# Kernel tuning notes

Measured on AMD Instinct MI355X. Metric: run time of the kernel, lower is better.

The kernel has to match this reference:

```python
import jax, jax.numpy as jnp
import numpy as np

NUM_HEADS = 4
D_K = 64
D_MODEL = NUM_HEADS * D_K  # 256
SEN_LEN = 8192
N_GROUPS = 4096
BASE_LEN = 64
N_EDGES = N_GROUPS * BASE_LEN  # 262144
PATH_LEN = 64


def setup_inputs() -> dict:
    rng = np.random.default_rng(0)
    key = jax.random.key(0)
    ks = jax.random.split(key, 16)

    # ragged group lengths, each >= 2, summing exactly to N_EDGES
    half = N_GROUPS // 2
    r = rng.integers(-(BASE_LEN - 2), BASE_LEN - 1, size=half)
    edge_len = np.concatenate([BASE_LEN + r, BASE_LEN - r]).astype(np.int64)
    assert edge_len.sum() == N_EDGES and edge_len.min() >= 2

    # distinct token ids; include src=0 and tar=1 so path_agg branches fire
    perm = rng.permutation(np.arange(2, SEN_LEN))[: N_GROUPS - 2]
    token_ids = np.concatenate([np.array([0, 1]), perm]).astype(np.int64)

    def w(k, shape):
        return jax.random.normal(k, shape, jnp.float32) / np.sqrt(shape[-1]).astype(np.float32)

    return {
        "path": jax.random.normal(ks[0], (PATH_LEN, D_MODEL), jnp.float32),
        "path_len": PATH_LEN,
        "q": jax.random.normal(ks[1], (SEN_LEN, D_MODEL), jnp.float32),
        "k": jax.random.normal(ks[2], (N_EDGES, D_MODEL), jnp.float32),
        "v": jax.random.normal(ks[3], (N_EDGES, D_MODEL), jnp.float32),
        "graphs": 0,
        "edge_len": jnp.asarray(edge_len),
        "token_ids": jnp.asarray(token_ids),
        "pair": jnp.array([0, 1], jnp.int32),
        "rev": 0,
        "W_qpair": w(ks[4], (D_MODEL, 2 * D_MODEL)),
        "W_pk": w(ks[5], (D_MODEL, D_MODEL)),
        "W_pv": w(ks[6], (D_MODEL, D_MODEL)),
        "W_q": w(ks[7], (D_MODEL, D_MODEL)),
        "W_k": w(ks[8], (D_MODEL, D_MODEL)),
        "W_v": w(ks[9], (D_MODEL, D_MODEL)),
        "W_out": w(ks[10], (D_MODEL, D_MODEL)),
        "b_out": jnp.zeros((D_MODEL,), jnp.float32),
        "W_agg": w(ks[11], (D_MODEL, 2 * D_MODEL)),
    }


def _forward(path, q, k, v, edge_len, token_ids, pair, rev,
             W_qpair, W_pk, W_pv, W_q, W_k, W_v, W_out, b_out, W_agg):
    H, dk = NUM_HEADS, D_K
    G = edge_len.shape[0]
    E = k.shape[0]
    scale = 1.0 / jnp.sqrt(jnp.float32(dk))

    src = pair[0] if rev == 0 else pair[1]
    tar = pair[1] if rev == 0 else pair[0]

    # pair query: cat(q[src], q[tar]) -> linear -> [H, 1, dk]
    pair_q = (jnp.concatenate([q[src], q[tar]]) @ W_qpair.T).reshape(1, H, dk).transpose(1, 0, 2)

    qh = (q @ W_q.T).reshape(-1, H, dk).transpose(1, 0, 2)      # [H, S, dk]
    pk = (path @ W_pk.T).reshape(-1, H, dk).transpose(1, 0, 2)  # [H, P, dk]
    pv = (path @ W_pv.T).reshape(-1, H, dk).transpose(1, 0, 2)  # [H, P, dk]
    kh = (k @ W_k.T).reshape(-1, H, dk).transpose(1, 0, 2)      # [H, E, dk]
    vh = (v @ W_v.T).reshape(-1, H, dk).transpose(1, 0, 2)      # [H, E, dk]

    # ---- pair/path attention ----
    att = jax.nn.softmax(jnp.einsum('hqd,hpd->hqp', pair_q, pk) * scale, axis=-1)  # [H,1,P]
    path_vals = jnp.einsum('hqp,hpd->hqd', att, pv).sum(axis=1)  # [H, dk]
    path_result = path_vals.reshape(-1) @ W_out.T + b_out        # [d_model]

    # ---- segmented per-group attention (vectorized ragged loop) ----
    seg = jnp.repeat(jnp.arange(G), edge_len, total_repeat_length=E)  # [E]
    q_sel = qh[:, token_ids, :]          # [H, G, dk] query per group
    qe = q_sel[:, seg, :]                # [H, E, dk] query per edge
    # torch.matmul(q_[H,dk], k_[H,i,dk].T) broadcasts to cross-head logits [a,b,i]
    logits = jnp.einsum('aed,bed->eab', qe, kh) * scale  # [E, H, H]
    lmax = jax.lax.stop_gradient(jax.ops.segment_max(logits, seg, num_segments=G))
    ex = jnp.exp(logits - lmax[seg])
    denom = jax.ops.segment_sum(ex, seg, num_segments=G)
    p = ex / denom[seg]                                   # segmented softmax [E, H, H]
    # sum over key-head b per edge, then segment-reduce over edges of each group
    out_e = jnp.einsum('eab,bed->ead', p, vh)             # [E, H, dk]
    hid = jax.ops.segment_sum(out_e, seg, num_segments=G) # [G, H, dk]
    new_hid = hid.reshape(G, H * dk) @ W_out.T + b_out    # [G, d_model] (dropout=identity)

    # ---- assemble output rows ----
    pr = jnp.broadcast_to(path_result, (G, D_MODEL))
    feat_path = jnp.concatenate([new_hid, pr], axis=1) @ W_agg.T  # token == src
    path_feat = jnp.concatenate([pr, new_hid], axis=1) @ W_agg.T  # token == tar
    is_src = (token_ids == src)[:, None]
    is_tar = (token_ids == tar)[:, None]
    vals = jnp.where(is_src, feat_path, jnp.where(is_tar, path_feat, new_hid))
    returned = q.at[token_ids].set(vals)
    return returned, att


def reference(path, path_len, q, k, v, graphs, edge_len, token_ids, pair, rev,
              W_qpair, W_pk, W_pv, W_q, W_k, W_v, W_out, b_out, W_agg):
    return _forward(path, q, k, v, edge_len, token_ids, pair, rev,
                    W_qpair, W_pk, W_pv, W_q, W_k, W_v, W_out, b_out, W_agg)
```

## Files before the change

### kernel.cpp

```cpp
#include <hip/hip_runtime.h>
#include <hip/hip_bf16.h>

#define H 4
#define DK 64
#define DM 256
#define SEN 8192
#define NG 4096
#define ETOT 262144
#define PLEN 64
#define MAXE 128

typedef unsigned short ushortT;
typedef __attribute__((ext_vector_type(8))) __bf16 bf16x8;
typedef __attribute__((ext_vector_type(8))) unsigned short us8;
typedef __attribute__((ext_vector_type(4))) unsigned short us4;
typedef __attribute__((ext_vector_type(4))) float f32x4;

#define TMS 264
#define KVS 260

__device__ __forceinline__ ushortT f2bf(float f) {
    unsigned u = __float_as_uint(f);
    u += 0x7FFF + ((u >> 16) & 1);
    return (ushortT)(u >> 16);
}
__device__ __forceinline__ bf16x8 ldb8(const ushortT* p) {
    us8 v = *(const us8*)p;
    return __builtin_bit_cast(bf16x8, v);
}
__device__ __forceinline__ bf16x8 pack8(const float* f) {
    us8 v;
#pragma unroll
    for (int j = 0; j < 8; j++) v[j] = f2bf(f[j]);
    return __builtin_bit_cast(bf16x8, v);
}
__device__ __forceinline__ ushortT sbf(float f) {
    return __builtin_bit_cast(ushortT, (__bf16)f);
}
__device__ __forceinline__ __bf16 u2b(ushortT u) {
    return __builtin_bit_cast(__bf16, u);
}
__device__ __forceinline__ bf16x8 pack8f(float4 a, float4 b) {
    bf16x8 r;
    r[0] = (__bf16)a.x; r[1] = (__bf16)a.y; r[2] = (__bf16)a.z; r[3] = (__bf16)a.w;
    r[4] = (__bf16)b.x; r[5] = (__bf16)b.y; r[6] = (__bf16)b.z; r[7] = (__bf16)b.w;
    return r;
}


__global__ __launch_bounds__(256) void prep_kernel(
    const float* __restrict__ q, float* __restrict__ out,
    const int* __restrict__ edge_len, int* __restrict__ starts,
    const float* __restrict__ path, const int* __restrict__ pair,
    const int* __restrict__ rev, const float* __restrict__ W_qpair,
    const float* __restrict__ W_pk, const float* __restrict__ W_pv,
    float* __restrict__ pv_ws, float* __restrict__ logits_ws,
    const float* __restrict__ W_q, const float* __restrict__ W_k,
    const float* __restrict__ W_v, const float* __restrict__ W_out,
    ushortT* __restrict__ WQb, ushortT* __restrict__ WKTb,
    ushortT* __restrict__ WVb, ushortT* __restrict__ WOb) {
    __shared__ int part[256];
    __shared__ float cat[512];
    __shared__ float pq[256];
    __shared__ float prow[256];
    __shared__ float lp[256];
    const int b = blockIdx.x;
    const int tid = threadIdx.x;
    if (b < 2048) {
        const size_t i = (size_t)b * 256 + tid;
        ((float4*)out)[i] = ((const float4*)q)[i];
    } else if (b < 3072) {
        const int idx = (b - 2048) * 256 + tid;
        const int sel = idx >> 16;
        const int i = idx & 65535;
        if (sel == 0) {
            WQb[i] = sbf(W_q[i]);
        } else if (sel == 1) {
            const int c = i >> 8, d = i & 255;
            WKTb[i] = sbf(W_k[d * DM + c]);
        } else if (sel == 2) {
            WVb[i] = sbf(W_v[i]);
        } else {
            WOb[i] = sbf(W_out[i]);
        }
    } else if (b == 3072) {
        const int base = tid * 16;
        int loc[16];
        int s = 0;
#pragma unroll
        for (int i = 0; i < 16; i++) { loc[i] = s; s += edge_len[base + i]; }
        part[tid] = s;
        __syncthreads();
        if (tid == 0) {
            int acc = 0;
            for (int i = 0; i < 256; i++) { int t = part[i]; part[i] = acc; acc += t; }
        }
        __syncthreads();
        const int off = part[tid];
#pragma unroll
        for (int i = 0; i < 16; i++) starts[base + i] = off + loc[i];
    } else {
        const int p = b - 3073;
        const int rv = rev[0];
        const int src = (rv == 0) ? pair[0] : pair[1];
        const int tar = (rv == 0) ? pair[1] : pair[0];
        cat[tid] = q[(size_t)src * DM + tid];
        cat[256 + tid] = q[(size_t)tar * DM + tid];
        prow[tid] = path[p * DM + tid];
        __syncthreads();
        float acc = 0.f;
        for (int c = 0; c < 512; c += 4) {
            float4 w4 = *(const float4*)&W_qpair[(size_t)tid * 512 + c];
            acc += w4.x * cat[c] + w4.y * cat[c + 1] + w4.z * cat[c + 2] + w4.w * cat[c + 3];
        }
        pq[tid] = acc;
        __syncthreads();
        float pkv = 0.f, pvv = 0.f;
        for (int c = 0; c < 256; c += 4) {
            float4 a4 = *(const float4*)&W_pk[tid * DM + c];
            float4 b4 = *(const float4*)&W_pv[tid * DM + c];
            float4 x4 = *(const float4*)&prow[c];
            pkv += a4.x * x4.x + a4.y * x4.y + a4.z * x4.z + a4.w * x4.w;
            pvv += b4.x * x4.x + b4.y * x4.y + b4.z * x4.z + b4.w * x4.w;
        }
        pv_ws[p * DM + tid] = pvv;
        lp[tid] = pq[tid] * pkv;
        __syncthreads();
        if (tid < H) {
            float s = 0.f;
            for (int d = 0; d < DK; d++) s += lp[tid * DK + d];
            logits_ws[tid * PLEN + p] = s * 0.125f;
        }
    }
}

__global__ __launch_bounds__(256) void qhtmatC_kernel(
    const float* __restrict__ q, const int* __restrict__ token_ids,
    const ushortT* __restrict__ WQb, const ushortT* __restrict__ WKTb,
    ushortT* __restrict__ tmat_u,
    const float* __restrict__ pv_ws, const float* __restrict__ logits_ws,
    const float* __restrict__ W_out, const float* __restrict__ b_out,
    float* __restrict__ att_out, float* __restrict__ path_result) {
    __shared__ ushortT Al[16 * 264];
    __shared__ ushortT QHs[16 * 264];
    __shared__ float att[256];
    __shared__ float pvals[256];
    const int tid = threadIdx.x;
    if (blockIdx.x == 256) {
        att[tid] = logits_ws[tid];
        __syncthreads();
        if (tid < H) {
            float m = -3.0e38f;
            for (int p = 0; p < PLEN; p++) m = fmaxf(m, att[tid * PLEN + p]);
            float s = 0.f;
            for (int p = 0; p < PLEN; p++) {
                float e = __expf(att[tid * PLEN + p] - m);
                att[tid * PLEN + p] = e;
                s += e;
            }
            float inv = 1.f / s;
            for (int p = 0; p < PLEN; p++) att[tid * PLEN + p] *= inv;
        }
        __syncthreads();
        att_out[tid] = att[tid];
        {
            const int h = tid >> 6;
            float a = 0.f;
            for (int p = 0; p < PLEN; p++) a += att[h * PLEN + p] * pv_ws[p * DM + tid];
            pvals[tid] = a;
        }
        __syncthreads();
        {
            float a = b_out[tid];
            for (int c = 0; c < 256; c += 4) {
                float4 w4 = *(const float4*)&W_out[tid * DM + c];
                a += w4.x * pvals[c] + w4.y * pvals[c + 1] + w4.z * pvals[c + 2] + w4.w * pvals[c + 3];
            }
            path_result[tid] = a;
        }
        return;
    }
    const int g0 = blockIdx.x * 16;
    const int lane = tid & 63, w = tid >> 6, lq = lane & 15, lh = lane >> 4;
    {
        const int m = tid >> 4;
        const int c0 = (tid & 15) * 16;
        const int tok = token_ids[g0 + m];
        const float* qr = &q[(size_t)tok * DM + c0];
#pragma unroll
        for (int i = 0; i < 4; i++) {
            float4 v4 = *(const float4*)&qr[i * 4];
            us4 o;
            o[0] = sbf(v4.x); o[1] = sbf(v4.y); o[2] = sbf(v4.z); o[3] = sbf(v4.w);
            *(us4*)&Al[m * 264 + c0 + i * 4] = o;
        }
    }
    __syncthreads();
    {
        bf16x8 af[8];
#pragma unroll
        for (int kk = 0; kk < 8; kk++) af[kk] = ldb8(&Al[lq * 264 + kk * 32 + lh * 8]);
#pragma unroll
        for (int ntl = 0; ntl < 4; ntl++) {
            const int nt = w * 4 + ntl;
            f32x4 acc = {0.f, 0.f, 0.f, 0.f};
#pragma unroll
            for (int kk = 0; kk < 8; kk++) {
                bf16x8 bf = ldb8(&WQb[(nt * 16 + lq) * 256 + kk * 32 + lh * 8]);
                acc = __builtin_amdgcn_mfma_f32_16x16x32_bf16(af[kk], bf, acc, 0, 0, 0);
            }
#pragma unroll
            for (int r = 0; r < 4; r++)
                QHs[(lh * 4 + r) * 264 + nt * 16 + lq] = sbf(acc[r]);
        }
    }
    __syncthreads();
    for (int ab = 0; ab < 16; ab++) {
        const int a = ab >> 2, bb = ab & 3;
        bf16x8 a0 = ldb8(&QHs[lq * 264 + a * 64 + lh * 8]);
        bf16x8 a1 = ldb8(&QHs[lq * 264 + a * 64 + 32 + lh * 8]);
#pragma unroll
        for (int ntl = 0; ntl < 4; ntl++) {
            const int nt = w * 4 + ntl;
            f32x4 acc = {0.f, 0.f, 0.f, 0.f};
            bf16x8 b0 = ldb8(&WKTb[(nt * 16 + lq) * 256 + bb * 64 + lh * 8]);
            acc = __builtin_amdgcn_mfma_f32_16x16x32_bf16(a0, b0, acc, 0, 0, 0);
            bf16x8 b1 = ldb8(&WKTb[(nt * 16 + lq) * 256 + bb * 64 + 32 + lh * 8]);
            acc = __builtin_amdgcn_mfma_f32_16x16x32_bf16(a1, b1, acc, 0, 0, 0);
#pragma unroll
            for (int r = 0; r < 4; r++)
                tmat_u[((size_t)(g0 + lh * 4 + r) * 16 + ab) * 256 + nt * 16 + lq] =
                    sbf(acc[r]);
        }
    }
}

__global__ __launch_bounds__(256, 3) void edge_kernel(
    const float* __restrict__ k, const float* __restrict__ v,
    const int* __restrict__ edge_len, const int* __restrict__ starts,
    ushortT* __restrict__ tmat_u) {
    const int g = blockIdx.x;
    const int tid = threadIdx.x;
    const float scale = 0.125f;
    __shared__ float plog[128][17];
    __shared__ ushortT pT[16 * 136];
    __shared__ float red[16][16];
    __shared__ float mx[16];
    __shared__ ushortT kvb[64 * KVS];
    const int start = starts[g];
    const int len = edge_len[g];
    const int lane = tid & 63, w = tid >> 6, lq = lane & 15, lh = lane >> 4;
    const int rg = tid >> 4, cc = tid & 15;
    const int nkc = (len + 31) >> 5;
    const int nmt = (len + 15) >> 4;
    const int col = (tid & 63) * 4;
    const int rr = tid >> 6;

    bf16x8 btm[8];
#pragma unroll
    for (int cb = 0; cb < 8; cb++)
        btm[cb] = ldb8(&tmat_u[((size_t)g * 16 + lq) * 256 + cb * 32 + lh * 8]);

    const int nch = (nmt + 3) >> 2;
    for (int c = 0; c < nch; c++) {
        const int base = c * 64;
        const int cnt = len - base;
        const int rquads = (cnt < 64 ? cnt + 3 : 67) >> 2;
#pragma unroll
        for (int i = 0; i < 16; i++) {
            if (i < rquads) {
                const int row = i * 4 + rr;
                const int gr = base + row;
                const int grc = (gr < len) ? gr : (len - 1);
                float4 v4 = *(const float4*)&k[(size_t)(start + grc) * DM + col];
                us4 o;
                o[0] = sbf(v4.x); o[1] = sbf(v4.y); o[2] = sbf(v4.z); o[3] = sbf(v4.w);
                *(us4*)&kvb[row * KVS + col] = o;
            }
        }
        __syncthreads();
        const int t = c * 4 + w;
        if (t < nmt) {
            f32x4 acc = {0.f, 0.f, 0.f, 0.f};
#pragma unroll
            for (int cb = 0; cb < 8; cb++) {
                bf16x8 ak = ldb8(&kvb[(w * 16 + lq) * KVS + cb * 32 + lh * 8]);
                acc = __builtin_amdgcn_mfma_f32_16x16x32_bf16(ak, btm[cb], acc, 0, 0, 0);
            }
#pragma unroll
            for (int r = 0; r < 4; r++) plog[t * 16 + lh * 4 + r][lq] = acc[r] * scale;
        }
        __syncthreads();
    }

    {
        float m = -3.0e38f;
        for (int e = rg; e < len; e += 16) m = fmaxf(m, plog[e][cc]);
        red[rg][cc] = m;
        __syncthreads();
        if (tid < 16) {
            float mm = red[0][tid];
            for (int i2 = 1; i2 < 16; i2++) mm = fmaxf(mm, red[i2][tid]);
            mx[tid] = mm;
        }
        __syncthreads();
        const float mm = mx[cc];
        float s = 0.f;
        for (int e = rg; e < len; e += 16) {
            float ex = __expf(plog[e][cc] - mm);
            plog[e][cc] = ex;
            s += ex;
        }
        red[rg][cc] = s;
        __syncthreads();
        if (tid < 16) {
            float ss = red[0][tid];
            for (int i2 = 1; i2 < 16; i2++) ss += red[i2][tid];
            mx[tid] = 1.0f / ss;
        }
        __syncthreads();
        const float inv = mx[cc];
        const int padlen = nkc * 32;
        for (int e = rg; e < padlen; e += 16) {
            float pv = (e < len) ? plog[e][cc] * inv : 0.f;
            pT[cc * 136 + e] = sbf(pv);
        }
    }
    __syncthreads();

    {
        f32x4 uacc[4];
#pragma unroll
        for (int nt = 0; nt < 4; nt++) uacc[nt] = {0.f, 0.f, 0.f, 0.f};
        for (int kc = 0; kc < nkc; kc++) {
            const int base = kc * 32;
#pragma unroll
            for (int i = 0; i < 8; i++) {
                const int row = i * 4 + rr;
                const int gr = base + row;
                const int grc = (gr < len) ? gr : (len - 1);
                float4 v4 = *(const float4*)&v[(size_t)(start + grc) * DM + col];
                us4 o;
                o[0] = sbf(v4.x); o[1] = sbf(v4.y); o[2] = sbf(v4.z); o[3] = sbf(v4.w);
                *(us4*)&kvb[row * KVS + col] = o;
            }
            __syncthreads();
            bf16x8 ap = ldb8(&pT[lq * 136 + kc * 32 + lh * 8]);
#pragma unroll
            for (int nt = 0; nt < 4; nt++) {
                bf16x8 bv;
#pragma unroll
                for (int j = 0; j < 8; j++)
                    bv[j] = u2b(kvb[(lh * 8 + j) * KVS + w * 64 + nt * 16 + lq]);
                uacc[nt] = __builtin_amdgcn_mfma_f32_16x16x32_bf16(ap, bv, uacc[nt], 0, 0, 0);
            }
            __syncthreads();
        }
        const int c0 = w * 64;
#pragma unroll
        for (int nt = 0; nt < 4; nt++) {
#pragma unroll
            for (int r = 0; r < 4; r++) {
                const int ab = lh * 4 + r;
                tmat_u[((size_t)g * 16 + ab) * 256 + c0 + nt * 16 + lq] = sbf(uacc[nt][r]);
            }
        }
    }
}

__global__ __launch_bounds__(256) void hidnhagg_kernel(
    const ushortT* __restrict__ Ub, const ushortT* __restrict__ WVb,
    const ushortT* __restrict__ WOb, const float* __restrict__ b_out,
    const int* __restrict__ token_ids, const int* __restrict__ pair,
    const int* __restrict__ rev, const float* __restrict__ W_agg,
    const float* __restrict__ path_result, float* __restrict__ out) {
    __shared__ ushortT HIDs[16 * 264];
    __shared__ float nhs[2][260];
    __shared__ float prb[256];
    __shared__ int flagrow[2];
    const int tid = threadIdx.x;
    const int g0 = blockIdx.x * 16;
    const int lane = tid & 63, w = tid >> 6, lq = lane & 15, lh = lane >> 4;
    if (tid < 2) flagrow[tid] = -1;
    prb[tid] = path_result[tid];
#pragma unroll
    for (int a = 0; a < 4; a++) {
        f32x4 acc = {0.f, 0.f, 0.f, 0.f};
        for (int kk = 0; kk < 32; kk++) {
            const int kbase = kk * 32 + lh * 8;
            bf16x8 af = ldb8(&Ub[((size_t)(g0 + lq) * 16 + a * 4) * 256 + kbase]);
            bf16x8 bf = ldb8(&WVb[(size_t)((kbase >> 8) * 64 + w * 16 + lq) * 256 + (kbase & 255)]);
            acc = __builtin_amdgcn_mfma_f32_16x16x32_bf16(af, bf, acc, 0, 0, 0);
        }
#pragma unroll
        for (int r = 0; r < 4; r++)
            HIDs[(lh * 4 + r) * 264 + a * 64 + w * 16 + lq] = sbf(acc[r]);
    }
    __syncthreads();
    bf16x8 af2[8];
#pragma unroll
    for (int kk = 0; kk < 8; kk++) af2[kk] = ldb8(&HIDs[lq * 264 + kk * 32 + lh * 8]);
    const int rv = rev[0];
    const int src = (rv == 0) ? pair[0] : pair[1];
    const int tar = (rv == 0) ? pair[1] : pair[0];
    int toks[4];
#pragma unroll
    for (int r = 0; r < 4; r++) {
        toks[r] = token_ids[g0 + lh * 4 + r];
        if (toks[r] == src) flagrow[0] = lh * 4 + r;
        else if (toks[r] == tar) flagrow[1] = lh * 4 + r;
    }
#pragma unroll
    for (int ntl = 0; ntl < 4; ntl++) {
        const int nt = w * 4 + ntl;
        f32x4 acc = {0.f, 0.f, 0.f, 0.f};
#pragma unroll
        for (int kk = 0; kk < 8; kk++) {
            bf16x8 bf = ldb8(&WOb[(nt * 16 + lq) * 256 + kk * 32 + lh * 8]);
            acc = __builtin_amdgcn_mfma_f32_16x16x32_bf16(af2[kk], bf, acc, 0, 0, 0);
        }
        const int n = nt * 16 + lq;
        const float bo = b_out[n];
#pragma unroll
        for (int r = 0; r < 4; r++) {
            const float val = acc[r] + bo;
            if (toks[r] == src) nhs[0][n] = val;
            else if (toks[r] == tar) nhs[1][n] = val;
            else out[(size_t)toks[r] * DM + n] = val;
        }
    }
    __syncthreads();
#pragma unroll
    for (int s = 0; s < 2; s++) {
        if (flagrow[s] >= 0) {
            const float* x1 = (s == 0) ? nhs[0] : prb;
            const float* x2 = (s == 0) ? prb : nhs[1];
            float acc = 0.f;
            for (int n = 0; n < 256; n += 4) {
                float4 w4 = *(const float4*)&W_agg[(size_t)tid * 512 + n];
                acc += w4.x * x1[n] + w4.y * x1[n + 1] + w4.z * x1[n + 2] + w4.w * x1[n + 3];
            }
            for (int n = 0; n < 256; n += 4) {
                float4 w4 = *(const float4*)&W_agg[(size_t)tid * 512 + 256 + n];
                acc += w4.x * x2[n] + w4.y * x2[n + 1] + w4.z * x2[n + 2] + w4.w * x2[n + 3];
            }
            out[(size_t)((s == 0) ? src : tar) * DM + tid] = acc;
        }
    }
}


__global__ __launch_bounds__(256) void scan_kernel(const int* __restrict__ edge_len,
                                                   int* __restrict__ starts) {
    __shared__ int part[256];
    const int tid = threadIdx.x;
    const int base = tid * 16;
    int loc[16];
    int s = 0;
#pragma unroll
    for (int i = 0; i < 16; i++) { loc[i] = s; s += edge_len[base + i]; }
    part[tid] = s;
    __syncthreads();
    if (tid == 0) {
        int acc = 0;
        for (int i = 0; i < 256; i++) { int t = part[i]; part[i] = acc; acc += t; }
    }
    __syncthreads();
    const int off = part[tid];
#pragma unroll
    for (int i = 0; i < 16; i++) starts[base + i] = off + loc[i];
}

__global__ void copy_kernel(const float* __restrict__ q, float* __restrict__ out) {
    const size_t i = (size_t)blockIdx.x * blockDim.x + threadIdx.x;
    ((float4*)out)[i] = ((const float4*)q)[i];
}

__global__ __launch_bounds__(256) void pathB_kernel(
    const float* __restrict__ path, const float* __restrict__ q,
    const int* __restrict__ pair, const int* __restrict__ rev,
    const float* __restrict__ W_qpair, const float* __restrict__ W_pk,
    const float* __restrict__ W_pv,
    float* __restrict__ pv_ws, float* __restrict__ logits_ws) {
    __shared__ float cat[512];
    __shared__ float pq[256];
    __shared__ float prow[256];
    __shared__ float lp[256];
    const int p = blockIdx.x;
    const int tid = threadIdx.x;
    const int rv = rev[0];
    const int src = (rv == 0) ? pair[0] : pair[1];
    const int tar = (rv == 0) ? pair[1] : pair[0];
    cat[tid] = q[(size_t)src * DM + tid];
    cat[256 + tid] = q[(size_t)tar * DM + tid];
    prow[tid] = path[p * DM + tid];
    __syncthreads();
    float acc = 0.f;
    for (int c = 0; c < 512; c += 4) {
        float4 w4 = *(const float4*)&W_qpair[(size_t)tid * 512 + c];
        acc += w4.x * cat[c] + w4.y * cat[c + 1] + w4.z * cat[c + 2] + w4.w * cat[c + 3];
    }
    pq[tid] = acc;
    __syncthreads();
    float pkv = 0.f, pvv = 0.f;
    for (int c = 0; c < 256; c += 4) {
        float4 a4 = *(const float4*)&W_pk[tid * DM + c];
        float4 b4 = *(const float4*)&W_pv[tid * DM + c];
        float4 x4 = *(const float4*)&prow[c];
        pkv += a4.x * x4.x + a4.y * x4.y + a4.z * x4.z + a4.w * x4.w;
        pvv += b4.x * x4.x + b4.y * x4.y + b4.z * x4.z + b4.w * x4.w;
    }
    pv_ws[p * DM + tid] = pvv;
    lp[tid] = pq[tid] * pkv;
    __syncthreads();
    if (tid < H) {
        float s = 0.f;
        for (int d = 0; d < DK; d++) s += lp[tid * DK + d];
        logits_ws[tid * PLEN + p] = s * 0.125f;
    }
}

__global__ __launch_bounds__(256) void pathC_kernel(
    const float* __restrict__ pv_ws, const float* __restrict__ logits_ws,
    const float* __restrict__ W_out, const float* __restrict__ b_out,
    float* __restrict__ att_out, float* __restrict__ path_result) {
    __shared__ float att[256];
    __shared__ float pvals[256];
    const int tid = threadIdx.x;
    att[tid] = logits_ws[tid];
    __syncthreads();
    if (tid < H) {
        float m = -3.0e38f;
        for (int p = 0; p < PLEN; p++) m = fmaxf(m, att[tid * PLEN + p]);
        float s = 0.f;
        for (int p = 0; p < PLEN; p++) {
            float e = __expf(att[tid * PLEN + p] - m);
            att[tid * PLEN + p] = e;
            s += e;
        }
        float inv = 1.f / s;
        for (int p = 0; p < PLEN; p++) att[tid * PLEN + p] *= inv;
    }
    __syncthreads();
    att_out[tid] = att[tid];
    {
        const int h = tid >> 6;
        float a = 0.f;
        for (int p = 0; p < PLEN; p++) a += att[h * PLEN + p] * pv_ws[p * DM + tid];
        pvals[tid] = a;
    }
    __syncthreads();
    {
        float a = b_out[tid];
        for (int c = 0; c < 256; c += 4) {
            float4 w4 = *(const float4*)&W_out[tid * DM + c];
            a += w4.x * pvals[c] + w4.y * pvals[c + 1] + w4.z * pvals[c + 2] + w4.w * pvals[c + 3];
        }
        path_result[tid] = a;
    }
}

__global__ __launch_bounds__(256, 4) void group_kernel(
    const float* __restrict__ q, const float* __restrict__ k, const float* __restrict__ v,
    const int* __restrict__ edge_len, const int* __restrict__ token_ids,
    const int* __restrict__ pair, const int* __restrict__ rev,
    const float* __restrict__ W_q,
    const float* __restrict__ W_k, const float* __restrict__ W_v,
    const float* __restrict__ W_out, const float* __restrict__ b_out,
    const float* __restrict__ W_agg,
    const int* __restrict__ starts, const float* __restrict__ path_result,
    float* __restrict__ out) {
    const int g = blockIdx.x;
    const int tid = threadIdx.x;
    const float scale = 0.125f;

    __shared__ float qrow[256];
    __shared__ float qh[256];
    __shared__ ushortT qh_b[4 * 72];
    __shared__ ushortT tmat_b[16 * TMS];
    __shared__ float plog[128][17];
    __shared__ ushortT pT[16 * 136];
    __shared__ ushortT u_b[4 * 1032];
    __shared__ float hid[256];
    __shared__ float nh[256];
    __shared__ float red[16][16];
    __shared__ float mx[16];

    const int tok = token_ids[g];
    const int start = starts[g];
    const int len = edge_len[g];

    const int lane = tid & 63;
    const int w = tid >> 6;
    const int lq = lane & 15;
    const int lh = lane >> 4;
    const int rg = tid >> 4;
    const int cc = tid & 15;

    qrow[tid] = q[(size_t)tok * DM + tid];
    __syncthreads();

    for (int i = 0; i < 16; i++) {
        const int r = i * 16 + rg;
        float acc = 0.f;
#pragma unroll
        for (int j4 = 0; j4 < 4; j4++) {
            const int c0 = j4 * 64 + cc * 4;
            float4 w4 = *(const float4*)&W_q[r * DM + c0];
            float4 x4 = *(const float4*)&qrow[c0];
            acc += w4.x * x4.x + w4.y * x4.y + w4.z * x4.z + w4.w * x4.w;
        }
#pragma unroll
        for (int off = 8; off; off >>= 1) acc += __shfl_down(acc, off, 16);
        if (cc == 0) qh[r] = acc;
    }
    __syncthreads();
    qh_b[(tid >> 6) * 72 + (tid & 63)] = f2bf(qh[tid]);
    __syncthreads();

    {
        const int arow = (lq < 3) ? lq : 3;
        bf16x8 aq0 = ldb8(&qh_b[arow * 72 + lh * 8]);
        bf16x8 aq1 = ldb8(&qh_b[arow * 72 + 32 + lh * 8]);
        for (int nt = 0; nt < 16; nt++) {
            const int c = nt * 16 + lq;
            f32x4 acc = {0.f, 0.f, 0.f, 0.f};
            float wf[8];
#pragma unroll
            for (int j = 0; j < 8; j++)
                wf[j] = W_k[(size_t)(w * 64 + lh * 8 + j) * DM + c];
            acc = __builtin_amdgcn_mfma_f32_16x16x32_bf16(aq0, pack8(wf), acc, 0, 0, 0);
#pragma unroll
            for (int j = 0; j < 8; j++)
                wf[j] = W_k[(size_t)(w * 64 + 32 + lh * 8 + j) * DM + c];
            acc = __builtin_amdgcn_mfma_f32_16x16x32_bf16(aq1, pack8(wf), acc, 0, 0, 0);
            if (lane < 16) {
#pragma unroll
                for (int r = 0; r < 4; r++)
                    tmat_b[(r * 4 + w) * TMS + nt * 16 + lq] = f2bf(acc[r]);
            }
        }
    }
    __syncthreads();

    {
        bf16x8 btm[8];
#pragma unroll
        for (int cb = 0; cb < 8; cb++)
            btm[cb] = ldb8(&tmat_b[lq * TMS + cb * 32 + lh * 8]);
        const int nmt = (len + 15) >> 4;
        for (int t = w; t < nmt; t += 4) {
            const int e = t * 16 + lq;
            const int ec = (e < len) ? e : (len - 1);
            const float* krow = &k[(size_t)(start + ec) * DM + lh * 8];
            f32x4 acc = {0.f, 0.f, 0.f, 0.f};
#pragma unroll
            for (int cb = 0; cb < 8; cb++) {
                float4 k0 = *(const float4*)&krow[cb * 32];
                float4 k1 = *(const float4*)&krow[cb * 32 + 4];
                float kf[8] = {k0.x, k0.y, k0.z, k0.w, k1.x, k1.y, k1.z, k1.w};
                acc = __builtin_amdgcn_mfma_f32_16x16x32_bf16(pack8(kf), btm[cb], acc, 0, 0, 0);
            }
#pragma unroll
            for (int r = 0; r < 4; r++) plog[t * 16 + lh * 4 + r][lq] = acc[r] * scale;
        }
    }
    __syncthreads();

    const int nkc = (len + 31) >> 5;
    {
        float m = -3.0e38f;
        for (int e = rg; e < len; e += 16) m = fmaxf(m, plog[e][cc]);
        red[rg][cc] = m;
        __syncthreads();
        if (tid < 16) {
            float mm = red[0][tid];
            for (int i2 = 1; i2 < 16; i2++) mm = fmaxf(mm, red[i2][tid]);
            mx[tid] = mm;
        }
        __syncthreads();
        const float mm = mx[cc];
        float s = 0.f;
        for (int e = rg; e < len; e += 16) {
            float ex = __expf(plog[e][cc] - mm);
            plog[e][cc] = ex;
            s += ex;
        }
        red[rg][cc] = s;
        __syncthreads();
        if (tid < 16) {
            float ss = red[0][tid];
            for (int i2 = 1; i2 < 16; i2++) ss += red[i2][tid];
            mx[tid] = 1.0f / ss;
        }
        __syncthreads();
        const float inv = mx[cc];
        const int padlen = nkc * 32;
        for (int e = rg; e < padlen; e += 16) {
            float pv = (e < len) ? plog[e][cc] * inv : 0.f;
            pT[cc * 136 + e] = f2bf(pv);
        }
    }
    __syncthreads();

    {
        f32x4 uacc[4];
#pragma unroll
        for (int nt = 0; nt < 4; nt++) uacc[nt] = {0.f, 0.f, 0.f, 0.f};
        const int c0 = w * 64;
#pragma unroll
        for (int kc = 0; kc < 4; kc++) {
            if (kc < nkc) {
                bf16x8 ap = ldb8(&pT[lq * 136 + kc * 32 + lh * 8]);
#pragma unroll
                for (int nt = 0; nt < 4; nt++) {
                    float bf[8];
#pragma unroll
                    for (int j = 0; j < 8; j++) {
                        int e = kc * 32 + lh * 8 + j;
                        int ecl = (e < len) ? e : (len - 1);
                        bf[j] = v[(size_t)(start + ecl) * DM + c0 + nt * 16 + lq];
                    }
                    uacc[nt] = __builtin_amdgcn_mfma_f32_16x16x32_bf16(ap, pack8(bf), uacc[nt], 0, 0, 0);
                }
            }
        }
#pragma unroll
        for (int nt = 0; nt < 4; nt++) {
#pragma unroll
            for (int r = 0; r < 4; r++) {
                const int row = lh * 4 + r;
                const int a = row >> 2, b = row & 3;
                u_b[a * 1032 + b * 256 + c0 + nt * 16 + lq] = f2bf(uacc[nt][r]);
            }
        }
    }
    __syncthreads();

    {
        const int arow = (lq < 3) ? lq : 3;
        f32x4 hacc = {0.f, 0.f, 0.f, 0.f};
        for (int kc = 0; kc < 32; kc++) {
            bf16x8 au = ldb8(&u_b[arow * 1032 + kc * 32 + lh * 8]);
            const int kk = kc * 32 + lh * 8;
            const float* wr = &W_v[(size_t)((kk >> 8) * 64 + w * 16 + lq) * DM + (kk & 255)];
            float4 w0 = *(const float4*)&wr[0];
            float4 w1 = *(const float4*)&wr[4];
            float wf[8] = {w0.x, w0.y, w0.z, w0.w, w1.x, w1.y, w1.z, w1.w};
            hacc = __builtin_amdgcn_mfma_f32_16x16x32_bf16(au, pack8(wf), hacc, 0, 0, 0);
        }
        if (lane < 16) {
#pragma unroll
            for (int r = 0; r < 4; r++) hid[r * 64 + w * 16 + lq] = hacc[r];
        }
    }
    __syncthreads();

    for (int i = 0; i < 16; i++) {
        const int m = i * 16 + rg;
        float acc = 0.f;
#pragma unroll
        for (int j4 = 0; j4 < 4; j4++) {
            const int c0 = j4 * 64 + cc * 4;
            float4 w4 = *(const float4*)&W_out[m * DM + c0];
            float4 h4 = *(const float4*)&hid[c0];
            acc += w4.x * h4.x + w4.y * h4.y + w4.z * h4.z + w4.w * h4.w;
        }
#pragma unroll
        for (int off = 8; off; off >>= 1) acc += __shfl_down(acc, off, 16);
        if (cc == 0) nh[m] = b_out[m] + acc;
    }
    __syncthreads();

    const int rv = rev[0];
    const int src = (rv == 0) ? pair[0] : pair[1];
    const int tar = (rv == 0) ? pair[1] : pair[0];
    float val;
    if (tok == src || tok == tar) {
        qrow[tid] = path_result[tid];
        __syncthreads();
        const float* x1 = (tok == src) ? nh : qrow;
        const float* x2 = (tok == src) ? qrow : nh;
        float acc = 0.f;
        for (int n = 0; n < 256; n += 4) {
            float4 w4 = *(const float4*)&W_agg[(size_t)tid * 512 + n];
            acc += w4.x * x1[n] + w4.y * x1[n + 1] + w4.z * x1[n + 2] + w4.w * x1[n + 3];
        }
        for (int n = 0; n < 256; n += 4) {
            float4 w4 = *(const float4*)&W_agg[(size_t)tid * 512 + 256 + n];
            acc += w4.x * x2[n] + w4.y * x2[n + 1] + w4.z * x2[n + 2] + w4.w * x2[n + 3];
        }
        val = acc;
    } else {
        val = nh[tid];
    }
    out[(size_t)tok * DM + tid] = val;
}

extern "C" void kernel_launch(void* const* d_in, const int* in_sizes, int n_in,
                              void* d_out, int out_size, void* d_ws, size_t ws_size,
                              hipStream_t stream) {
    const float* path    = (const float*)d_in[0];
    const float* q       = (const float*)d_in[2];
    const float* k       = (const float*)d_in[3];
    const float* v       = (const float*)d_in[4];
    const int*   edge_len  = (const int*)d_in[6];
    const int*   token_ids = (const int*)d_in[7];
    const int*   pair      = (const int*)d_in[8];
    const int*   rev       = (const int*)d_in[9];
    const float* W_qpair = (const float*)d_in[10];
    const float* W_pk    = (const float*)d_in[11];
    const float* W_pv    = (const float*)d_in[12];
    const float* W_q     = (const float*)d_in[13];
    const float* W_k     = (const float*)d_in[14];
    const float* W_v     = (const float*)d_in[15];
    const float* W_out   = (const float*)d_in[16];
    const float* b_out   = (const float*)d_in[17];
    const float* W_agg   = (const float*)d_in[18];
    float* out = (float*)d_out;

    char* base = (char*)d_ws;
    int*    starts      = (int*)(base + 0);
    float*  path_result = (float*)(base + 16384);
    float*  pv_ws       = (float*)(base + 17408);
    float*  logits_ws   = (float*)(base + 82944);
    ushortT* WQb        = (ushortT*)(base + 83968);
    ushortT* WKTb       = (ushortT*)(base + 215040);
    ushortT* WVb        = (ushortT*)(base + 346112);
    ushortT* WOb        = (ushortT*)(base + 477184);
    ushortT* tmat_u     = (ushortT*)(base + 608256);
    const size_t NEED = 608256 + 33554432;

    if (ws_size >= NEED) {
        prep_kernel<<<dim3(3137), dim3(256), 0, stream>>>(
            q, out, edge_len, starts, path, pair, rev, W_qpair, W_pk, W_pv,
            pv_ws, logits_ws, W_q, W_k, W_v, W_out, WQb, WKTb, WVb, WOb);
        qhtmatC_kernel<<<dim3(257), dim3(256), 0, stream>>>(
            q, token_ids, WQb, WKTb, tmat_u, pv_ws, logits_ws, W_out, b_out,
            out + (size_t)SEN * DM, path_result);
        edge_kernel<<<dim3(NG), dim3(256), 0, stream>>>(k, v, edge_len, starts, tmat_u);
        hidnhagg_kernel<<<dim3(256), dim3(256), 0, stream>>>(
            tmat_u, WVb, WOb, b_out, token_ids, pair, rev, W_agg, path_result, out);
    } else {
        copy_kernel<<<dim3(2048), dim3(256), 0, stream>>>(q, out);
        scan_kernel<<<dim3(1), dim3(256), 0, stream>>>(edge_len, starts);
        pathB_kernel<<<dim3(PLEN), dim3(256), 0, stream>>>(path, q, pair, rev, W_qpair,
                                                           W_pk, W_pv, pv_ws, logits_ws);
        pathC_kernel<<<dim3(1), dim3(256), 0, stream>>>(pv_ws, logits_ws, W_out, b_out,
                                                        out + (size_t)SEN * DM, path_result);
        group_kernel<<<dim3(NG), dim3(256), 0, stream>>>(q, k, v, edge_len, token_ids, pair,
                                                         rev, W_q, W_k, W_v, W_out, b_out,
                                                         W_agg, starts, path_result, out);
    }
}
```

Baseline: 301.4 us.

## Load K/V tiles directly into LDS as fp32 via global_load_lds

Replaces the register-staged K and V loads, which converted to bf16 before writing to LDS, with direct global-to-LDS 16-byte loads of fp32 rows. The bf16 conversion moves to the consumer side, after the LDS read. The K phase now uses 32-row chunks computed by only two of the four waves, which halves MFMA parallelism in that phase. The goal is to save VGPRs and the conversion work in the load path, but the LDS traffic doubles and more loop iterations are needed. The row pitch of 260 floats in the LDS destination may also not match how global_load_lds writes contiguously per wave.

```diff
diff --git a/kernel.cpp b/kernel.cpp
--- a/kernel.cpp
+++ b/kernel.cpp
@@ -17,7 +17,7 @@
 typedef __attribute__((ext_vector_type(4))) float f32x4;
 
 #define TMS 264
-#define KVS 260
+#define KVSF 260
 
 __device__ __forceinline__ ushortT f2bf(float f) {
     unsigned u = __float_as_uint(f);
@@ -36,15 +36,17 @@
 }
 __device__ __forceinline__ ushortT sbf(float f) {
     return __builtin_bit_cast(ushortT, (__bf16)f);
-}
-__device__ __forceinline__ __bf16 u2b(ushortT u) {
-    return __builtin_bit_cast(__bf16, u);
 }
 __device__ __forceinline__ bf16x8 pack8f(float4 a, float4 b) {
     bf16x8 r;
     r[0] = (__bf16)a.x; r[1] = (__bf16)a.y; r[2] = (__bf16)a.z; r[3] = (__bf16)a.w;
     r[4] = (__bf16)b.x; r[5] = (__bf16)b.y; r[6] = (__bf16)b.z; r[7] = (__bf16)b.w;
     return r;
+}
+__device__ __forceinline__ void gload_row16(const float* g, float* lds) {
+    __builtin_amdgcn_global_load_lds(
+        (const __attribute__((address_space(1))) void*)g,
+        (__attribute__((address_space(3))) void*)lds, 16, 0, 0);
 }
 
 
@@ -246,46 +248,36 @@
     __shared__ ushortT pT[16 * 136];
     __shared__ float red[16][16];
     __shared__ float mx[16];
-    __shared__ ushortT kvb[64 * KVS];
+    __shared__ float kvf[32 * KVSF];
     const int start = starts[g];
     const int len = edge_len[g];
     const int lane = tid & 63, w = tid >> 6, lq = lane & 15, lh = lane >> 4;
     const int rg = tid >> 4, cc = tid & 15;
     const int nkc = (len + 31) >> 5;
     const int nmt = (len + 15) >> 4;
-    const int col = (tid & 63) * 4;
-    const int rr = tid >> 6;
 
     bf16x8 btm[8];
 #pragma unroll
     for (int cb = 0; cb < 8; cb++)
         btm[cb] = ldb8(&tmat_u[((size_t)g * 16 + lq) * 256 + cb * 32 + lh * 8]);
 
-    const int nch = (nmt + 3) >> 2;
-    for (int c = 0; c < nch; c++) {
-        const int base = c * 64;
-        const int cnt = len - base;
-        const int rquads = (cnt < 64 ? cnt + 3 : 67) >> 2;
-#pragma unroll
-        for (int i = 0; i < 16; i++) {
-            if (i < rquads) {
-                const int row = i * 4 + rr;
-                const int gr = base + row;
-                const int grc = (gr < len) ? gr : (len - 1);
-                float4 v4 = *(const float4*)&k[(size_t)(start + grc) * DM + col];
-                us4 o;
-                o[0] = sbf(v4.x); o[1] = sbf(v4.y); o[2] = sbf(v4.z); o[3] = sbf(v4.w);
-                *(us4*)&kvb[row * KVS + col] = o;
-            }
-        }
-        __syncthreads();
-        const int t = c * 4 + w;
-        if (t < nmt) {
+    for (int c = 0; c < nkc; c++) {
+#pragma unroll
+        for (int i = 0; i < 8; i++) {
+            const int row = i * 4 + w;
+            const int gr = c * 32 + row;
+            const int grc = (gr < len) ? gr : (len - 1);
+            gload_row16(&k[(size_t)(start + grc) * DM + lane * 4], &kvf[row * KVSF]);
+        }
+        __syncthreads();
+        const int t = c * 2 + w;
+        if (w < 2 && t < nmt) {
             f32x4 acc = {0.f, 0.f, 0.f, 0.f};
 #pragma unroll
             for (int cb = 0; cb < 8; cb++) {
-                bf16x8 ak = ldb8(&kvb[(w * 16 + lq) * KVS + cb * 32 + lh * 8]);
-                acc = __builtin_amdgcn_mfma_f32_16x16x32_bf16(ak, btm[cb], acc, 0, 0, 0);
+                float4 f0 = *(const float4*)&kvf[(w * 16 + lq) * KVSF + cb * 32 + lh * 8];
+                float4 f1 = *(const float4*)&kvf[(w * 16 + lq) * KVSF + cb * 32 + lh * 8 + 4];
+                acc = __builtin_amdgcn_mfma_f32_16x16x32_bf16(pack8f(f0, f1), btm[cb], acc, 0, 0, 0);
             }
 #pragma unroll
             for (int r = 0; r < 4; r++) plog[t * 16 + lh * 4 + r][lq] = acc[r] * scale;
@@ -333,16 +325,12 @@
 #pragma unroll
         for (int nt = 0; nt < 4; nt++) uacc[nt] = {0.f, 0.f, 0.f, 0.f};
         for (int kc = 0; kc < nkc; kc++) {
-            const int base = kc * 32;
 #pragma unroll
             for (int i = 0; i < 8; i++) {
-                const int row = i * 4 + rr;
-                const int gr = base + row;
+                const int row = i * 4 + w;
+                const int gr = kc * 32 + row;
                 const int grc = (gr < len) ? gr : (len - 1);
-                float4 v4 = *(const float4*)&v[(size_t)(start + grc) * DM + col];
-                us4 o;
-                o[0] = sbf(v4.x); o[1] = sbf(v4.y); o[2] = sbf(v4.z); o[3] = sbf(v4.w);
-                *(us4*)&kvb[row * KVS + col] = o;
+                gload_row16(&v[(size_t)(start + grc) * DM + lane * 4], &kvf[row * KVSF]);
             }
             __syncthreads();
             bf16x8 ap = ldb8(&pT[lq * 136 + kc * 32 + lh * 8]);
@@ -351,7 +339,7 @@
                 bf16x8 bv;
 #pragma unroll
                 for (int j = 0; j < 8; j++)
-                    bv[j] = u2b(kvb[(lh * 8 + j) * KVS + w * 64 + nt * 16 + lq]);
+                    bv[j] = (__bf16)kvf[(lh * 8 + j) * KVSF + w * 64 + nt * 16 + lq];
                 uacc[nt] = __builtin_amdgcn_mfma_f32_16x16x32_bf16(ap, bv, uacc[nt], 0, 0, 0);
             }
             __syncthreads();
```

Result: faster. 273.1 us (-9.4%).
